# Optimization experiments

Hardware: AMD Instinct MI355X
Metric: run time of the kernel (lower is better)

The kernel has to match this reference:

```python
import jax, jax.numpy as jnp
import numpy as np

B = 512        # number of graphs
NPG = 128      # nodes per graph
N = B * NPG    # total nodes = 65536
E = 262144     # total edges (intra-graph)
F_IN = 128     # input features
H = 256        # hidden
C = 2          # num classes
BN_EPS = 1e-5


def _lin_params(key, fan_in, fan_out):
    k1, k2 = jax.random.split(key)
    s = 1.0 / np.sqrt(fan_in)
    w = jax.random.uniform(k1, (fan_in, fan_out), jnp.float32, -s, s)
    b = jax.random.uniform(k2, (fan_out,), jnp.float32, -s, s)
    return w, b


def setup_inputs() -> dict:
    key = jax.random.key(0)
    ks = jax.random.split(key, 16)
    x = jax.random.normal(ks[0], (N, F_IN), jnp.float32)
    # intra-graph random edges (required for assignment pooling semantics)
    rng = np.random.RandomState(0)
    g = np.repeat(np.arange(B), E // B)
    src = g * NPG + rng.randint(0, NPG, E)
    dst = g * NPG + rng.randint(0, NPG, E)
    edge_index = jnp.asarray(np.stack([src, dst]), jnp.int64 if jax.config.jax_enable_x64 else jnp.int32)
    batch = jnp.repeat(jnp.arange(B), NPG)
    # GIN layer 0 (F_IN->H->H) + BN
    w0_1, b0_1 = _lin_params(ks[1], F_IN, H)
    w0_2, b0_2 = _lin_params(ks[2], H, H)
    g0 = jnp.ones((H,), jnp.float32); be0 = jnp.zeros((H,), jnp.float32)
    # GIN layers 1..2 stacked (H->H->H) + BN
    wl1 = jnp.stack([_lin_params(jax.random.fold_in(ks[3], i), H, H)[0] for i in range(2)])
    bl1 = jnp.stack([_lin_params(jax.random.fold_in(ks[3], i), H, H)[1] for i in range(2)])
    wl2 = jnp.stack([_lin_params(jax.random.fold_in(ks[4], i), H, H)[0] for i in range(2)])
    bl2 = jnp.stack([_lin_params(jax.random.fold_in(ks[4], i), H, H)[1] for i in range(2)])
    gl = jnp.ones((2, H), jnp.float32); bel = jnp.zeros((2, H), jnp.float32)
    c1w, c1b = _lin_params(ks[5], H, H)
    c2w, c2b = _lin_params(ks[6], H, 2)
    l1w, l1b = _lin_params(ks[7], H, H)
    l2w, l2b = _lin_params(ks[8], H, C)
    return dict(x=x, edge_index=edge_index, batch=batch,
                w0_1=w0_1, b0_1=b0_1, w0_2=w0_2, b0_2=b0_2, g0=g0, be0=be0,
                wl1=wl1, bl1=bl1, wl2=wl2, bl2=bl2, gl=gl, bel=bel,
                c1w=c1w, c1b=c1b, c2w=c2w, c2b=c2b,
                l1w=l1w, l1b=l1b, l2w=l2w, l2b=l2b)


def _gin_layer(h, src, dst, w1, b1, w2, b2, gamma, beta):
    # GINConv (eps=0): MLP(h + sum_{j in N(i)} h_j)
    agg = jax.ops.segment_sum(h[src], dst, num_segments=N)
    z = h + agg
    z = jax.nn.relu(z @ w1 + b1)
    z = jax.nn.relu(z @ w2 + b2)
    # BatchNorm1d, training-mode batch stats (biased variance)
    mu = jnp.mean(z, axis=0)
    var = jnp.mean((z - mu) ** 2, axis=0)
    return (z - mu) * jax.lax.rsqrt(var + BN_EPS) * gamma + beta


def reference(x, edge_index, batch, w0_1, b0_1, w0_2, b0_2, g0, be0,
              wl1, bl1, wl2, bl2, gl, bel,
              c1w, c1b, c2w, c2b, l1w, l1b, l2w, l2b):
    src, dst = edge_index[0], edge_index[1]
    h = _gin_layer(x, src, dst, w0_1, b0_1, w0_2, b0_2, g0, be0)
    for i in range(2):
        h = _gin_layer(h, src, dst, wl1[i], bl1[i], wl2[i], bl2[i], gl[i], bel[i])
    # assignment: softmax(cluster2(tanh(cluster1(h))))  -> [N, 2]
    a = jax.nn.softmax(jnp.tanh(h @ c1w + c1b) @ c2w + c2b, axis=1)
    # subgraph embedding: (assignment^T @ x)[0] per graph == segment-sum of a[:,0]*h
    sub = jax.ops.segment_sum(a[:, :1] * h, batch, num_segments=B)        # [B, H]
    # graph embedding: per-graph mean of h
    cnt = jax.ops.segment_sum(jnp.ones((N,), h.dtype), batch, num_segments=B)
    graph = jax.ops.segment_sum(h, batch, num_segments=B) / cnt[:, None]   # [B, H]
    # new_adj[g] = A_g^T-pooled: sum over edges outer(a[src], a[dst]) -> [B,2,2]
    new_adj = jax.ops.segment_sum(a[src][:, :, None] * a[dst][:, None, :], batch[src], num_segments=B)
    # F.normalize(p=1, dim=1) row-wise, then diagonal, MSE vs ones(2)
    rown = jnp.maximum(jnp.sum(jnp.abs(new_adj), axis=2, keepdims=True), 1e-12)
    norm_adj = new_adj / rown
    diag = jnp.diagonal(norm_adj, axis1=1, axis2=2)                        # [B, 2]
    con_penalty = jnp.mean(jnp.mean((diag - 1.0) ** 2, axis=1))
    # classifier head (dropout in eval mode -> identity)
    z = jax.nn.relu(sub @ l1w + l1b)
    out = jax.nn.log_softmax(z @ l2w + l2b, axis=-1)
    return out, sub, graph, con_penalty
```

## Files before the change

kernel.cpp:

```cpp
#include <hip/hip_runtime.h>
#include <stdint.h>

#define NN 65536
#define NB 512
#define NPG 128
#define NE 262144
#define EPG 512
#define HD 256
#define BN_EPS 1e-5f

typedef unsigned short u16;
typedef float f32x4 __attribute__((ext_vector_type(4)));
typedef __bf16 bf16x8 __attribute__((ext_vector_type(8)));
typedef unsigned short u16x8 __attribute__((ext_vector_type(8)));
typedef unsigned short u16x4 __attribute__((ext_vector_type(4)));

__device__ __forceinline__ float b2f(u16 u){
  union { unsigned i; float f; } x; x.i = ((unsigned)u) << 16; return x.f;
}
__device__ __forceinline__ u16 f2b(float f){
  union { float f; unsigned i; } x; x.f = f;
  unsigned r = x.i + 0x7fffu + ((x.i >> 16) & 1u);
  return (u16)(r >> 16);
}
__device__ __forceinline__ float ftanh(float x){
  float e = __expf(2.0f * x);
  return 1.0f - 2.0f * __builtin_amdgcn_rcpf(e + 1.0f);
}

__global__ void __launch_bounds__(256) pack_all(
    const float* __restrict__ w0_1, const float* __restrict__ w0_2,
    const float* __restrict__ wl1, const float* __restrict__ wl2,
    const float* __restrict__ c1w,
    u16* i01, u16* i02, u16* il1a, u16* il1b, u16* il2a, u16* il2b, u16* ic1)
{
  const int seg = blockIdx.y;
  const int idx = blockIdx.x * 256 + threadIdx.x;
  const float* W; u16* img; int K = 256;
  switch (seg){
    case 0: W = w0_1;        img = i01;  K = 128; break;
    case 1: W = w0_2;        img = i02;  break;
    case 2: W = wl1;         img = il1a; break;
    case 3: W = wl1 + 65536; img = il1b; break;
    case 4: W = wl2;         img = il2a; break;
    case 5: W = wl2 + 65536; img = il2b; break;
    default: W = c1w;        img = ic1;  break;
  }
  if (idx >= K * 256) return;
  int col = idx / K, k = idx - col * K;
  img[idx] = f2b(W[(size_t)k * 256 + col]);
}

template<int K>
__device__ __forceinline__ void mm_frag(const u16* Alds,
    const u16* __restrict__ wimg, int lane, int c0, f32x4 (&acc)[8][2])
{
  const int l15 = lane & 15, lk = (lane >> 4) * 8;
  bf16x8 bfr[K / 32][2];
  #pragma unroll
  for (int kk = 0; kk < K / 32; kk++)
    #pragma unroll
    for (int nf = 0; nf < 2; nf++)
      bfr[kk][nf] = *(const bf16x8*)(wimg + (size_t)(c0 + nf * 16 + l15) * K + kk * 32 + lk);
  #pragma unroll
  for (int kk = 0; kk < K / 32; kk++){
    bf16x8 af[8];
    #pragma unroll
    for (int mf = 0; mf < 8; mf++){
      int row = mf * 16 + l15;
      unsigned byte = ((unsigned)(row * (K * 2) + (kk * 32 + lk) * 2)) ^ (unsigned)((row & 7) << 4);
      af[mf] = *(const bf16x8*)((const char*)Alds + byte);
    }
    #pragma unroll
    for (int mf = 0; mf < 8; mf++)
      #pragma unroll
      for (int nf = 0; nf < 2; nf++)
        acc[mf][nf] = __builtin_amdgcn_mfma_f32_16x16x32_bf16(af[mf], bfr[kk][nf], acc[mf][nf], 0, 0, 0);
  }
}

template<int KIN, int MODE>
__global__ void __launch_bounds__(512) layer_kernel(
    const void* __restrict__ hin_, const int* __restrict__ ei,
    const float* __restrict__ sc, const float* __restrict__ sh,
    const u16* __restrict__ w1img, const float* __restrict__ b1,
    const u16* __restrict__ w2img, const float* __restrict__ b2,
    u16* __restrict__ Y, float* __restrict__ pS, float* __restrict__ pQ)
{
  __shared__ u16 ht[NPG * HD];
  __shared__ u16 esd[EPG];
  __shared__ u16 srcs[EPG];
  __shared__ int cnt[NPG], rp[NPG + 1], fill[NPG];
  __shared__ float scs[256], shs[256];
  const int g = blockIdx.x, tid = threadIdx.x;
  const int lane = tid & 63, wid = tid >> 6;

  if (tid < NPG) cnt[tid] = 0;
  if (MODE == 1 && tid < 256){ scs[tid] = sc[tid]; shs[tid] = sh[tid]; }
  __syncthreads();

  {
    int s = ei[g * EPG + tid] & (NPG - 1);
    int d = ei[NE + g * EPG + tid] & (NPG - 1);
    esd[tid] = (u16)(s | (d << 8));
    atomicAdd(&cnt[d], 1);
  }

  if constexpr (MODE == 0){
    const float* hin = (const float*)hin_;
    #pragma unroll
    for (int i = 0; i < 8; i++){
      int idx = tid + i * 512;
      int row = idx >> 5, c4 = idx & 31;
      float4 v = *(const float4*)(hin + (size_t)(g * NPG + row) * KIN + c4 * 4);
      u16x4 o; o[0] = f2b(v.x); o[1] = f2b(v.y); o[2] = f2b(v.z); o[3] = f2b(v.w);
      unsigned byte = ((unsigned)(row * (KIN * 2) + c4 * 8)) ^ (unsigned)((row & 7) << 4);
      *(u16x4*)((char*)ht + byte) = o;
    }
  } else {
    const u16* hin = (const u16*)hin_;
    #pragma unroll
    for (int i = 0; i < 8; i++){
      int idx = tid + i * 512;
      int row = idx >> 5, c8 = idx & 31;
      u16x8 v = *(const u16x8*)(hin + (size_t)(g * NPG + row) * KIN + c8 * 8);
      u16x8 o;
      #pragma unroll
      for (int k = 0; k < 8; k++) o[k] = f2b(b2f(v[k]) * scs[c8 * 8 + k] + shs[c8 * 8 + k]);
      unsigned byte = ((unsigned)(row * (KIN * 2) + c8 * 16)) ^ (unsigned)((row & 7) << 4);
      *(u16x8*)((char*)ht + byte) = o;
    }
  }
  __syncthreads();

  if (tid < 64){
    int a = cnt[tid], b = cnt[tid + 64];
    int ca = a, cb = b;
    #pragma unroll
    for (int off = 1; off < 64; off <<= 1){
      int ta = __shfl_up(a, off), tb = __shfl_up(b, off);
      if (lane >= off){ a += ta; b += tb; }
    }
    int atot = __shfl(a, 63);
    rp[tid + 1] = a;
    rp[tid + 65] = atot + b;
    fill[tid] = a - ca;
    fill[tid + 64] = atot + b - cb;
    if (tid == 0) rp[0] = 0;
  }
  __syncthreads();
  { int v = esd[tid]; int pos = atomicAdd(&fill[v >> 8], 1); srcs[pos] = (u16)(v & 255); }
  __syncthreads();

  constexpr int CH = KIN / 16;
  constexpr int RPT = NPG * CH / 512;
  const int fc = tid & (CH - 1), n0 = tid / CH;
  float accv[RPT][16];
  #pragma unroll
  for (int j = 0; j < RPT; j++){
    const int n = n0 + j * (512 / CH);
    unsigned b0 = ((unsigned)(n * (KIN * 2) + fc * 32)) ^ (unsigned)((n & 7) << 4);
    u16x8 a0 = *(const u16x8*)((const char*)ht + b0);
    u16x8 a1 = *(const u16x8*)((const char*)ht + (b0 ^ 16u));
    #pragma unroll
    for (int k = 0; k < 8; k++){ accv[j][k] = b2f(a0[k]); accv[j][8 + k] = b2f(a1[k]); }
    const int e0 = rp[n], e1 = rp[n + 1];
    for (int e = e0; e < e1; e++){
      const int sn = srcs[e];
      unsigned s0 = ((unsigned)(sn * (KIN * 2) + fc * 32)) ^ (unsigned)((sn & 7) << 4);
      u16x8 q0 = *(const u16x8*)((const char*)ht + s0);
      u16x8 q1 = *(const u16x8*)((const char*)ht + (s0 ^ 16u));
      #pragma unroll
      for (int k = 0; k < 8; k++){ accv[j][k] += b2f(q0[k]); accv[j][8 + k] += b2f(q1[k]); }
    }
  }
  __syncthreads();
  #pragma unroll
  for (int j = 0; j < RPT; j++){
    const int n = n0 + j * (512 / CH);
    u16x8 o0, o1;
    #pragma unroll
    for (int k = 0; k < 8; k++){ o0[k] = f2b(accv[j][k]); o1[k] = f2b(accv[j][8 + k]); }
    unsigned b0 = ((unsigned)(n * (KIN * 2) + fc * 32)) ^ (unsigned)((n & 7) << 4);
    *(u16x8*)((char*)ht + b0) = o0;
    *(u16x8*)((char*)ht + (b0 ^ 16u)) = o1;
  }
  __syncthreads();

  const int c0 = wid * 32;
  const int l15 = lane & 15;

  {
    f32x4 acc1[8][2] = {};
    mm_frag<KIN>(ht, w1img, lane, c0, acc1);
    __syncthreads();
    float bv0 = b1[c0 + l15], bv1 = b1[c0 + 16 + l15];
    #pragma unroll
    for (int mf = 0; mf < 8; mf++)
      #pragma unroll
      for (int nf = 0; nf < 2; nf++){
        float bv = nf ? bv1 : bv0;
        int col = c0 + nf * 16 + l15;
        #pragma unroll
        for (int j = 0; j < 4; j++){
          int row = mf * 16 + (lane >> 4) * 4 + j;
          float v = fmaxf(acc1[mf][nf][j] + bv, 0.f);
          unsigned byte = ((unsigned)(row * 512 + col * 2)) ^ (unsigned)((row & 7) << 4);
          *(u16*)((char*)ht + byte) = f2b(v);
        }
      }
  }
  __syncthreads();

  {
    f32x4 acc2[8][2] = {};
    mm_frag<HD>(ht, w2img, lane, c0, acc2);
    float bv0 = b2[c0 + l15], bv1 = b2[c0 + 16 + l15];
    float s[2] = {0, 0}, q[2] = {0, 0};
    #pragma unroll
    for (int mf = 0; mf < 8; mf++)
      #pragma unroll
      for (int nf = 0; nf < 2; nf++){
        float bv = nf ? bv1 : bv0;
        int col = c0 + nf * 16 + l15;
        #pragma unroll
        for (int j = 0; j < 4; j++){
          int row = mf * 16 + (lane >> 4) * 4 + j;
          float v = fmaxf(acc2[mf][nf][j] + bv, 0.f);
          Y[(size_t)(g * NPG + row) * HD + col] = f2b(v);
          s[nf] += v; q[nf] += v * v;
        }
      }
    #pragma unroll
    for (int nf = 0; nf < 2; nf++){
      float sv = s[nf], qv = q[nf];
      sv += __shfl_xor(sv, 16); sv += __shfl_xor(sv, 32);
      qv += __shfl_xor(qv, 16); qv += __shfl_xor(qv, 32);
      if (lane < 16){
        int col = c0 + nf * 16 + lane;
        pS[(size_t)col * NB + g] = sv;
        pQ[(size_t)col * NB + g] = qv;
      }
    }
  }
}

__global__ void __launch_bounds__(64) bnfin_kernel(const float* __restrict__ pS,
    const float* __restrict__ pQ, const float* __restrict__ gma,
    const float* __restrict__ bta, float* __restrict__ scale, float* __restrict__ shift)
{
  int c = blockIdx.x, lane = threadIdx.x;
  float s = 0.f, q = 0.f;
  for (int i = lane; i < NB; i += 64){ s += pS[(size_t)c * NB + i]; q += pQ[(size_t)c * NB + i]; }
  for (int m = 32; m; m >>= 1){ s += __shfl_xor(s, m); q += __shfl_xor(q, m); }
  if (lane == 0){
    float mu = s * (1.0f / NN);
    float var = q * (1.0f / NN) - mu * mu;
    float scv = gma[c] * rsqrtf(var + BN_EPS);
    scale[c] = scv;
    shift[c] = bta[c] - mu * scv;
  }
}

__global__ void __launch_bounds__(512) final_kernel(
    const u16* __restrict__ hin, const int* __restrict__ ei,
    const float* __restrict__ sc, const float* __restrict__ sh,
    const u16* __restrict__ c1img, const float* __restrict__ c1b,
    const float* __restrict__ c2w, const float* __restrict__ c2b,
    const float* __restrict__ l1w, const float* __restrict__ l1b,
    const float* __restrict__ l2w, const float* __restrict__ l2b,
    float* __restrict__ outLog, float* __restrict__ outSub,
    float* __restrict__ outGraph, float* __restrict__ outPen)
{
  __shared__ u16 ht[NPG * HD];
  __shared__ u16 esd[EPG];
  __shared__ float aL[NPG * 2];
  __shared__ float scratch[2048];
  __shared__ float subL[256];
  __shared__ float wred[8][4];
  const int g = blockIdx.x, tid = threadIdx.x;
  const int lane = tid & 63, wid = tid >> 6;

  if (tid < 256){ scratch[tid] = sc[tid]; scratch[256 + tid] = sh[tid]; }
  {
    int s = ei[g * EPG + tid] & (NPG - 1);
    int d = ei[NE + g * EPG + tid] & (NPG - 1);
    esd[tid] = (u16)(s | (d << 8));
  }
  __syncthreads();

  #pragma unroll
  for (int i = 0; i < 8; i++){
    int idx = tid + i * 512;
    int row = idx >> 5, c8 = idx & 31;
    u16x8 v = *(const u16x8*)(hin + (size_t)(g * NPG + row) * HD + c8 * 8);
    u16x8 o;
    #pragma unroll
    for (int k = 0; k < 8; k++)
      o[k] = f2b(b2f(v[k]) * scratch[c8 * 8 + k] + scratch[256 + c8 * 8 + k]);
    unsigned byte = ((unsigned)(row * 512 + c8 * 16)) ^ (unsigned)((row & 7) << 4);
    *(u16x8*)((char*)ht + byte) = o;
  }
  __syncthreads();

  const int c0 = wid * 32;
  const int l15 = lane & 15;

  {
    f32x4 acct[8][2] = {};
    mm_frag<HD>(ht, c1img, lane, c0, acct);
    const int col0 = c0 + l15, col1 = c0 + 16 + l15;
    const float bv0 = c1b[col0], bv1 = c1b[col1];
    const float w00 = c2w[col0 * 2], w01 = c2w[col0 * 2 + 1];
    const float w10 = c2w[col1 * 2], w11 = c2w[col1 * 2 + 1];
    #pragma unroll
    for (int mf = 0; mf < 8; mf++)
      #pragma unroll
      for (int j = 0; j < 4; j++){
        float t0 = ftanh(acct[mf][0][j] + bv0);
        float t1 = ftanh(acct[mf][1][j] + bv1);
        float p0 = t0 * w00 + t1 * w10;
        float p1 = t0 * w01 + t1 * w11;
        p0 += __shfl_xor(p0, 1); p0 += __shfl_xor(p0, 2);
        p0 += __shfl_xor(p0, 4); p0 += __shfl_xor(p0, 8);
        p1 += __shfl_xor(p1, 1); p1 += __shfl_xor(p1, 2);
        p1 += __shfl_xor(p1, 4); p1 += __shfl_xor(p1, 8);
        if (l15 == 0){
          int row = mf * 16 + (lane >> 4) * 4 + j;
          scratch[row * 16 + wid * 2]     = p0;
          scratch[row * 16 + wid * 2 + 1] = p1;
        }
      }
  }
  __syncthreads();

  {
    int row = tid >> 2, part = tid & 3;
    float4 v = *(const float4*)&scratch[row * 16 + part * 4];
    float p0 = v.x + v.z, p1 = v.y + v.w;
    p0 += __shfl_xor(p0, 1); p0 += __shfl_xor(p0, 2);
    p1 += __shfl_xor(p1, 1); p1 += __shfl_xor(p1, 2);
    if (part == 0){
      p0 += c2b[0]; p1 += c2b[1];
      float mx = fmaxf(p0, p1);
      float e0 = expf(p0 - mx), e1 = expf(p1 - mx);
      float inv = 1.f / (e0 + e1);
      aL[row * 2] = e0 * inv; aL[row * 2 + 1] = e1 * inv;
    }
  }
  __syncthreads();

  {
    int v = esd[tid];
    int sE = v & 255, dE = v >> 8;
    float as0 = aL[sE * 2], as1 = aL[sE * 2 + 1];
    float ad0 = aL[dE * 2], ad1 = aL[dE * 2 + 1];
    float m00 = as0 * ad0, m01 = as0 * ad1, m10 = as1 * ad0, m11 = as1 * ad1;
    #pragma unroll
    for (int m = 1; m < 64; m <<= 1){
      m00 += __shfl_xor(m00, m); m01 += __shfl_xor(m01, m);
      m10 += __shfl_xor(m10, m); m11 += __shfl_xor(m11, m);
    }
    if (lane == 0){ wred[wid][0] = m00; wred[wid][1] = m01; wred[wid][2] = m10; wred[wid][3] = m11; }
  }
  {
    const int part = tid >> 8, c = tid & 255;
    float sb = 0.f, gs = 0.f;
    #pragma unroll 8
    for (int i = 0; i < 64; i++){
      int n = part * 64 + i;
      unsigned byte = ((unsigned)(n * 512 + c * 2)) ^ (unsigned)((n & 7) << 4);
      float v = b2f(*(const u16*)((const char*)ht + byte));
      sb += aL[n * 2] * v; gs += v;
    }
    __syncthreads();
    scratch[part * 512 + c] = sb;
    scratch[part * 512 + 256 + c] = gs;
  }
  __syncthreads();
  if (tid < 256){
    float sb = scratch[tid] + scratch[512 + tid];
    float gs = scratch[256 + tid] + scratch[768 + tid];
    subL[tid] = sb;
    outSub[(size_t)g * HD + tid] = sb;
    outGraph[(size_t)g * HD + tid] = gs * (1.f / NPG);
  }
  if (tid == 0){
    float m00 = 0, m01 = 0, m10 = 0, m11 = 0;
    for (int w = 0; w < 8; w++){ m00 += wred[w][0]; m01 += wred[w][1]; m10 += wred[w][2]; m11 += wred[w][3]; }
    float r0 = fmaxf(fabsf(m00) + fabsf(m01), 1e-12f);
    float r1 = fmaxf(fabsf(m10) + fabsf(m11), 1e-12f);
    float d0 = m00 / r0 - 1.f, d1 = m11 / r1 - 1.f;
    atomicAdd(outPen, 0.5f * (d0 * d0 + d1 * d1) * (1.0f / NB));
  }
  __syncthreads();

  {
    const int ph = tid >> 8, c = tid & 255;
    float z = 0.f;
    for (int k = ph * 128; k < ph * 128 + 128; k++)
      z += subL[k] * l1w[(size_t)k * HD + c];
    scratch[ph * 256 + c] = z;
  }
  __syncthreads();
  if (tid < 256){
    float z = fmaxf(scratch[tid] + scratch[256 + tid] + l1b[tid], 0.f);
    float o0 = z * l2w[tid * 2], o1 = z * l2w[tid * 2 + 1];
    #pragma unroll
    for (int m = 1; m < 64; m <<= 1){ o0 += __shfl_xor(o0, m); o1 += __shfl_xor(o1, m); }
    if (lane == 0){ wred[wid][0] = o0; wred[wid][1] = o1; }
  }
  __syncthreads();
  if (tid == 0){
    float o0 = wred[0][0] + wred[1][0] + wred[2][0] + wred[3][0] + l2b[0];
    float o1 = wred[0][1] + wred[1][1] + wred[2][1] + wred[3][1] + l2b[1];
    float mx = fmaxf(o0, o1);
    float lse = mx + logf(expf(o0 - mx) + expf(o1 - mx));
    outLog[(size_t)g * 2] = o0 - lse;
    outLog[(size_t)g * 2 + 1] = o1 - lse;
  }
}

extern "C" void kernel_launch(void* const* d_in, const int* in_sizes, int n_in,
                              void* d_out, int out_size, void* d_ws, size_t ws_size,
                              hipStream_t stream)
{
  (void)in_sizes; (void)n_in; (void)out_size; (void)ws_size;
  const float* x    = (const float*)d_in[0];
  const int*   ei   = (const int*)  d_in[1];
  const float* w0_1 = (const float*)d_in[3];
  const float* b0_1 = (const float*)d_in[4];
  const float* w0_2 = (const float*)d_in[5];
  const float* b0_2 = (const float*)d_in[6];
  const float* g0   = (const float*)d_in[7];
  const float* be0  = (const float*)d_in[8];
  const float* wl1  = (const float*)d_in[9];
  const float* bl1  = (const float*)d_in[10];
  const float* wl2  = (const float*)d_in[11];
  const float* bl2  = (const float*)d_in[12];
  const float* gl   = (const float*)d_in[13];
  const float* bel  = (const float*)d_in[14];
  const float* c1w  = (const float*)d_in[15];
  const float* c1b  = (const float*)d_in[16];
  const float* c2w  = (const float*)d_in[17];
  const float* c2b  = (const float*)d_in[18];
  const float* l1w  = (const float*)d_in[19];
  const float* l1b  = (const float*)d_in[20];
  const float* l2w  = (const float*)d_in[21];
  const float* l2b  = (const float*)d_in[22];
  float* out = (float*)d_out;

  char* cur = (char*)d_ws;
  auto carve = [&](size_t bytes) -> void* {
    void* p = (void*)cur; cur += (bytes + 255) & ~(size_t)255; return p;
  };
  u16* B0    = (u16*)carve((size_t)NN * HD * 2);
  u16* B1    = (u16*)carve((size_t)NN * HD * 2);
  u16* i01   = (u16*)carve((size_t)128 * 256 * 2);
  u16* i02   = (u16*)carve((size_t)256 * 256 * 2);
  u16* il1a  = (u16*)carve((size_t)256 * 256 * 2);
  u16* il1b  = (u16*)carve((size_t)256 * 256 * 2);
  u16* il2a  = (u16*)carve((size_t)256 * 256 * 2);
  u16* il2b  = (u16*)carve((size_t)256 * 256 * 2);
  u16* ic1   = (u16*)carve((size_t)256 * 256 * 2);
  float* pS  = (float*)carve((size_t)256 * NB * 4);
  float* pQ  = (float*)carve((size_t)256 * NB * 4);
  float* bsc = (float*)carve(256 * 4);
  float* bsh = (float*)carve(256 * 4);

  float* outPen = out + 1024 + 2 * NB * HD;

  pack_all<<<dim3(256, 7), 256, 0, stream>>>(w0_1, w0_2, wl1, wl2, c1w,
                                             i01, i02, il1a, il1b, il2a, il2b, ic1);
  hipMemsetAsync((void*)outPen, 0, 4, stream);

  layer_kernel<128, 0><<<NB, 512, 0, stream>>>((const void*)x, ei, nullptr, nullptr,
                                               i01, b0_1, i02, b0_2, B0, pS, pQ);
  bnfin_kernel<<<256, 64, 0, stream>>>(pS, pQ, g0, be0, bsc, bsh);

  layer_kernel<256, 1><<<NB, 512, 0, stream>>>((const void*)B0, ei, bsc, bsh,
                                               il1a, bl1, il2a, bl2, B1, pS, pQ);
  bnfin_kernel<<<256, 64, 0, stream>>>(pS, pQ, gl, bel, bsc, bsh);

  layer_kernel<256, 1><<<NB, 512, 0, stream>>>((const void*)B1, ei, bsc, bsh,
                                               il1b, bl1 + 256, il2b, bl2 + 256, B0, pS, pQ);
  bnfin_kernel<<<256, 64, 0, stream>>>(pS, pQ, gl + 256, bel + 256, bsc, bsh);

  final_kernel<<<NB, 512, 0, stream>>>(B0, ei, bsc, bsh, ic1, c1b, c2w, c2b,
                                       l1w, l1b, l2w, l2b,
                                       out, out + 1024, out + 1024 + NB * HD, outPen);
}
```

Baseline: 288.2 us.

## Replace CSR edge aggregation with dense adjacency MFMA after first linear

The layer kernel now builds a per-graph 128x128 dense adjacency (self-loop included) as 8-bit counts in LDS via atomics, instead of building CSR and gathering neighbours with scalar loops. Because aggregation commutes with the linear layer, it applies W1 first, then multiplies by the adjacency on MFMA, then adds bias and ReLU before the second GEMM. This removes the serial, divergent per-edge gather loops and the prefix-scan syncs. In exchange it adds extra MFMA work and a larger LDS footprint, and it requests two blocks per CU. The 8-bit counts overflow if any node pair has more than 255 edges, and rounding the W1 output to bf16 before aggregation changes numerics slightly.

```diff
diff --git a/kernel.cpp b/kernel.cpp
--- a/kernel.cpp
+++ b/kernel.cpp
@@ -26,6 +26,18 @@
 __device__ __forceinline__ float ftanh(float x){
   float e = __expf(2.0f * x);
   return 1.0f - 2.0f * __builtin_amdgcn_rcpf(e + 1.0f);
+}
+__device__ __forceinline__ bf16x8 u8x8_to_bf16x8(unsigned d0, unsigned d1){
+  u16x8 r;
+  #pragma unroll
+  for (int b = 0; b < 4; b++){
+    union { float f; unsigned u; } x, y;
+    x.f = (float)((d0 >> (b * 8)) & 255u);
+    y.f = (float)((d1 >> (b * 8)) & 255u);
+    r[b] = (u16)(x.u >> 16);
+    r[4 + b] = (u16)(y.u >> 16);
+  }
+  return *(bf16x8*)&r;
 }
 
 __global__ void __launch_bounds__(256) pack_all(
@@ -51,196 +63,223 @@
   img[idx] = f2b(W[(size_t)k * 256 + col]);
 }
 
-template<int K>
-__device__ __forceinline__ void mm_frag(const u16* Alds,
-    const u16* __restrict__ wimg, int lane, int c0, f32x4 (&acc)[8][2])
-{
-  const int l15 = lane & 15, lk = (lane >> 4) * 8;
-  bf16x8 bfr[K / 32][2];
-  #pragma unroll
-  for (int kk = 0; kk < K / 32; kk++)
-    #pragma unroll
-    for (int nf = 0; nf < 2; nf++)
-      bfr[kk][nf] = *(const bf16x8*)(wimg + (size_t)(c0 + nf * 16 + l15) * K + kk * 32 + lk);
-  #pragma unroll
-  for (int kk = 0; kk < K / 32; kk++){
-    bf16x8 af[8];
-    #pragma unroll
-    for (int mf = 0; mf < 8; mf++){
-      int row = mf * 16 + l15;
-      unsigned byte = ((unsigned)(row * (K * 2) + (kk * 32 + lk) * 2)) ^ (unsigned)((row & 7) << 4);
-      af[mf] = *(const bf16x8*)((const char*)Alds + byte);
-    }
-    #pragma unroll
-    for (int mf = 0; mf < 8; mf++)
-      #pragma unroll
-      for (int nf = 0; nf < 2; nf++)
-        acc[mf][nf] = __builtin_amdgcn_mfma_f32_16x16x32_bf16(af[mf], bfr[kk][nf], acc[mf][nf], 0, 0, 0);
-  }
-}
-
 template<int KIN, int MODE>
-__global__ void __launch_bounds__(512) layer_kernel(
+__global__ void __launch_bounds__(512, 2) layer_kernel(
     const void* __restrict__ hin_, const int* __restrict__ ei,
     const float* __restrict__ sc, const float* __restrict__ sh,
     const u16* __restrict__ w1img, const float* __restrict__ b1,
     const u16* __restrict__ w2img, const float* __restrict__ b2,
     u16* __restrict__ Y, float* __restrict__ pS, float* __restrict__ pQ)
 {
-  __shared__ u16 ht[NPG * HD];
-  __shared__ u16 esd[EPG];
-  __shared__ u16 srcs[EPG];
-  __shared__ int cnt[NPG], rp[NPG + 1], fill[NPG];
-  __shared__ float scs[256], shs[256];
+  __shared__ __align__(16) char smem[KIN * 256 + 65536 + 16384];
+  char* ht  = smem;
+  char* g1t = smem + KIN * 256;
+  unsigned* A32 = (unsigned*)(smem + KIN * 256 + 65536);
+  char* Ab = (char*)A32;
+
   const int g = blockIdx.x, tid = threadIdx.x;
   const int lane = tid & 63, wid = tid >> 6;
-
-  if (tid < NPG) cnt[tid] = 0;
-  if (MODE == 1 && tid < 256){ scs[tid] = sc[tid]; shs[tid] = sh[tid]; }
+  const int l15 = lane & 15, lk = (lane >> 4) * 8;
+  const int c0 = wid * 32;
+
+  #pragma unroll
+  for (int i = 0; i < 8; i++) A32[tid + i * 512] = 0u;
   __syncthreads();
 
   {
     int s = ei[g * EPG + tid] & (NPG - 1);
     int d = ei[NE + g * EPG + tid] & (NPG - 1);
-    esd[tid] = (u16)(s | (d << 8));
-    atomicAdd(&cnt[d], 1);
+    unsigned byte = ((unsigned)((d << 7) | (s & ~3))) ^ ((unsigned)((d & 7) << 4));
+    atomicAdd(&A32[byte >> 2], 1u << ((s & 3) * 8));
+  }
+  if (tid < NPG){
+    int n = tid;
+    unsigned byte = ((unsigned)((n << 7) | (n & ~3))) ^ ((unsigned)((n & 7) << 4));
+    atomicAdd(&A32[byte >> 2], 1u << ((n & 3) * 8));
   }
 
   if constexpr (MODE == 0){
     const float* hin = (const float*)hin_;
     #pragma unroll
+    for (int i = 0; i < 4; i++){
+      int idx = tid + i * 512;
+      int row = idx >> 4, c8 = idx & 15;
+      const float* p = hin + (size_t)(g * NPG + row) * KIN + c8 * 8;
+      float4 v0 = *(const float4*)p;
+      float4 v1 = *(const float4*)(p + 4);
+      u16x8 o;
+      o[0] = f2b(v0.x); o[1] = f2b(v0.y); o[2] = f2b(v0.z); o[3] = f2b(v0.w);
+      o[4] = f2b(v1.x); o[5] = f2b(v1.y); o[6] = f2b(v1.z); o[7] = f2b(v1.w);
+      unsigned byte = ((unsigned)(row * (KIN * 2) + c8 * 16)) ^ ((unsigned)((row & 7) << 4));
+      *(u16x8*)(ht + byte) = o;
+    }
+  } else {
+    const u16* hin = (const u16*)hin_;
+    const int c8 = tid & 31;
+    float scr[8], shr[8];
+    {
+      float4 a0 = *(const float4*)(sc + c8 * 8);
+      float4 a1 = *(const float4*)(sc + c8 * 8 + 4);
+      float4 s0 = *(const float4*)(sh + c8 * 8);
+      float4 s1 = *(const float4*)(sh + c8 * 8 + 4);
+      scr[0]=a0.x; scr[1]=a0.y; scr[2]=a0.z; scr[3]=a0.w;
+      scr[4]=a1.x; scr[5]=a1.y; scr[6]=a1.z; scr[7]=a1.w;
+      shr[0]=s0.x; shr[1]=s0.y; shr[2]=s0.z; shr[3]=s0.w;
+      shr[4]=s1.x; shr[5]=s1.y; shr[6]=s1.z; shr[7]=s1.w;
+    }
+    #pragma unroll
     for (int i = 0; i < 8; i++){
       int idx = tid + i * 512;
-      int row = idx >> 5, c4 = idx & 31;
-      float4 v = *(const float4*)(hin + (size_t)(g * NPG + row) * KIN + c4 * 4);
-      u16x4 o; o[0] = f2b(v.x); o[1] = f2b(v.y); o[2] = f2b(v.z); o[3] = f2b(v.w);
-      unsigned byte = ((unsigned)(row * (KIN * 2) + c4 * 8)) ^ (unsigned)((row & 7) << 4);
-      *(u16x4*)((char*)ht + byte) = o;
-    }
-  } else {
-    const u16* hin = (const u16*)hin_;
-    #pragma unroll
-    for (int i = 0; i < 8; i++){
-      int idx = tid + i * 512;
-      int row = idx >> 5, c8 = idx & 31;
+      int row = idx >> 5;
       u16x8 v = *(const u16x8*)(hin + (size_t)(g * NPG + row) * KIN + c8 * 8);
       u16x8 o;
       #pragma unroll
-      for (int k = 0; k < 8; k++) o[k] = f2b(b2f(v[k]) * scs[c8 * 8 + k] + shs[c8 * 8 + k]);
-      unsigned byte = ((unsigned)(row * (KIN * 2) + c8 * 16)) ^ (unsigned)((row & 7) << 4);
-      *(u16x8*)((char*)ht + byte) = o;
-    }
-  }
-  __syncthreads();
-
-  if (tid < 64){
-    int a = cnt[tid], b = cnt[tid + 64];
-    int ca = a, cb = b;
-    #pragma unroll
-    for (int off = 1; off < 64; off <<= 1){
-      int ta = __shfl_up(a, off), tb = __shfl_up(b, off);
-      if (lane >= off){ a += ta; b += tb; }
-    }
-    int atot = __shfl(a, 63);
-    rp[tid + 1] = a;
-    rp[tid + 65] = atot + b;
-    fill[tid] = a - ca;
-    fill[tid + 64] = atot + b - cb;
-    if (tid == 0) rp[0] = 0;
-  }
-  __syncthreads();
-  { int v = esd[tid]; int pos = atomicAdd(&fill[v >> 8], 1); srcs[pos] = (u16)(v & 255); }
-  __syncthreads();
-
-  constexpr int CH = KIN / 16;
-  constexpr int RPT = NPG * CH / 512;
-  const int fc = tid & (CH - 1), n0 = tid / CH;
-  float accv[RPT][16];
-  #pragma unroll
-  for (int j = 0; j < RPT; j++){
-    const int n = n0 + j * (512 / CH);
-    unsigned b0 = ((unsigned)(n * (KIN * 2) + fc * 32)) ^ (unsigned)((n & 7) << 4);
-    u16x8 a0 = *(const u16x8*)((const char*)ht + b0);
-    u16x8 a1 = *(const u16x8*)((const char*)ht + (b0 ^ 16u));
-    #pragma unroll
-    for (int k = 0; k < 8; k++){ accv[j][k] = b2f(a0[k]); accv[j][8 + k] = b2f(a1[k]); }
-    const int e0 = rp[n], e1 = rp[n + 1];
-    for (int e = e0; e < e1; e++){
-      const int sn = srcs[e];
-      unsigned s0 = ((unsigned)(sn * (KIN * 2) + fc * 32)) ^ (unsigned)((sn & 7) << 4);
-      u16x8 q0 = *(const u16x8*)((const char*)ht + s0);
-      u16x8 q1 = *(const u16x8*)((const char*)ht + (s0 ^ 16u));
-      #pragma unroll
-      for (int k = 0; k < 8; k++){ accv[j][k] += b2f(q0[k]); accv[j][8 + k] += b2f(q1[k]); }
-    }
-  }
-  __syncthreads();
-  #pragma unroll
-  for (int j = 0; j < RPT; j++){
-    const int n = n0 + j * (512 / CH);
-    u16x8 o0, o1;
-    #pragma unroll
-    for (int k = 0; k < 8; k++){ o0[k] = f2b(accv[j][k]); o1[k] = f2b(accv[j][8 + k]); }
-    unsigned b0 = ((unsigned)(n * (KIN * 2) + fc * 32)) ^ (unsigned)((n & 7) << 4);
-    *(u16x8*)((char*)ht + b0) = o0;
-    *(u16x8*)((char*)ht + (b0 ^ 16u)) = o1;
-  }
-  __syncthreads();
-
-  const int c0 = wid * 32;
-  const int l15 = lane & 15;
-
-  {
-    f32x4 acc1[8][2] = {};
-    mm_frag<KIN>(ht, w1img, lane, c0, acc1);
+      for (int k = 0; k < 8; k++) o[k] = f2b(b2f(v[k]) * scr[k] + shr[k]);
+      unsigned byte = ((unsigned)(row * (KIN * 2) + c8 * 16)) ^ ((unsigned)((row & 7) << 4));
+      *(u16x8*)(ht + byte) = o;
+    }
+  }
+  __syncthreads();
+
+  {
+    f32x4 acc[8][2] = {};
+    #pragma unroll
+    for (int kk = 0; kk < KIN / 32; kk++){
+      bf16x8 bfr[2];
+      #pragma unroll
+      for (int nf = 0; nf < 2; nf++)
+        bfr[nf] = *(const bf16x8*)(w1img + (size_t)(c0 + nf * 16 + l15) * KIN + kk * 32 + lk);
+      bf16x8 af[8];
+      #pragma unroll
+      for (int mf = 0; mf < 8; mf++){
+        int row = mf * 16 + l15;
+        unsigned byte = ((unsigned)(row * (KIN * 2) + (kk * 32 + lk) * 2)) ^ ((unsigned)((row & 7) << 4));
+        af[mf] = *(const bf16x8*)(ht + byte);
+      }
+      #pragma unroll
+      for (int mf = 0; mf < 8; mf++)
+        #pragma unroll
+        for (int nf = 0; nf < 2; nf++)
+          acc[mf][nf] = __builtin_amdgcn_mfma_f32_16x16x32_bf16(af[mf], bfr[nf], acc[mf][nf], 0, 0, 0);
+    }
+    #pragma unroll
+    for (int mf = 0; mf < 8; mf++)
+      #pragma unroll
+      for (int nf = 0; nf < 2; nf++){
+        int c = c0 + nf * 16 + l15;
+        int n0 = mf * 16 + (lane >> 4) * 4;
+        u16x4 o;
+        #pragma unroll
+        for (int j = 0; j < 4; j++) o[j] = f2b(acc[mf][nf][j]);
+        unsigned byte = ((unsigned)(c * 256 + n0 * 2)) ^ ((unsigned)((c & 7) << 4));
+        *(u16x4*)(g1t + byte) = o;
+      }
+  }
+
+  {
+    f32x4 acc[8][2] = {};
+    bf16x8 gfr[4][2];
+    #pragma unroll
+    for (int kk = 0; kk < 4; kk++)
+      #pragma unroll
+      for (int cf = 0; cf < 2; cf++){
+        int c = c0 + cf * 16 + l15;
+        unsigned byte = ((unsigned)(c * 256 + (kk * 32 + lk) * 2)) ^ ((unsigned)((c & 7) << 4));
+        gfr[kk][cf] = *(const bf16x8*)(g1t + byte);
+      }
+    #pragma unroll
+    for (int kk = 0; kk < 4; kk++){
+      bf16x8 bfA[8];
+      #pragma unroll
+      for (int nf = 0; nf < 8; nf++){
+        int n = nf * 16 + l15;
+        unsigned byte = ((unsigned)((n << 7) + kk * 32 + lk)) ^ ((unsigned)((n & 7) << 4));
+        uint2 dd = *(const uint2*)(Ab + byte);
+        bfA[nf] = u8x8_to_bf16x8(dd.x, dd.y);
+      }
+      #pragma unroll
+      for (int nf = 0; nf < 8; nf++)
+        #pragma unroll
+        for (int cf = 0; cf < 2; cf++)
+          acc[nf][cf] = __builtin_amdgcn_mfma_f32_16x16x32_bf16(gfr[kk][cf], bfA[nf], acc[nf][cf], 0, 0, 0);
+    }
     __syncthreads();
-    float bv0 = b1[c0 + l15], bv1 = b1[c0 + 16 + l15];
-    #pragma unroll
-    for (int mf = 0; mf < 8; mf++)
-      #pragma unroll
-      for (int nf = 0; nf < 2; nf++){
-        float bv = nf ? bv1 : bv0;
-        int col = c0 + nf * 16 + l15;
+    #pragma unroll
+    for (int nf = 0; nf < 8; nf++)
+      #pragma unroll
+      for (int cf = 0; cf < 2; cf++){
+        int n = nf * 16 + l15;
+        int cb = c0 + cf * 16 + (lane >> 4) * 4;
+        float4 bv = *(const float4*)(b1 + cb);
+        u16x4 o;
+        o[0] = f2b(fmaxf(acc[nf][cf][0] + bv.x, 0.f));
+        o[1] = f2b(fmaxf(acc[nf][cf][1] + bv.y, 0.f));
+        o[2] = f2b(fmaxf(acc[nf][cf][2] + bv.z, 0.f));
+        o[3] = f2b(fmaxf(acc[nf][cf][3] + bv.w, 0.f));
+        unsigned byte = ((unsigned)(n * 512 + cb * 2)) ^ ((unsigned)((n & 7) << 4));
+        *(u16x4*)(g1t + byte) = o;
+      }
+  }
+  __syncthreads();
+
+  {
+    f32x4 acc[8][2] = {};
+    #pragma unroll
+    for (int kk = 0; kk < 8; kk++){
+      bf16x8 bfr[2];
+      #pragma unroll
+      for (int cf = 0; cf < 2; cf++)
+        bfr[cf] = *(const bf16x8*)(w2img + (size_t)(c0 + cf * 16 + l15) * 256 + kk * 32 + lk);
+      bf16x8 zf[8];
+      #pragma unroll
+      for (int nf = 0; nf < 8; nf++){
+        int n = nf * 16 + l15;
+        unsigned byte = ((unsigned)(n * 512 + (kk * 32 + lk) * 2)) ^ ((unsigned)((n & 7) << 4));
+        zf[nf] = *(const bf16x8*)(g1t + byte);
+      }
+      #pragma unroll
+      for (int nf = 0; nf < 8; nf++)
+        #pragma unroll
+        for (int cf = 0; cf < 2; cf++)
+          acc[nf][cf] = __builtin_amdgcn_mfma_f32_16x16x32_bf16(bfr[cf], zf[nf], acc[nf][cf], 0, 0, 0);
+    }
+    float sv[2][4] = {}, qv[2][4] = {};
+    #pragma unroll
+    for (int nf = 0; nf < 8; nf++)
+      #pragma unroll
+      for (int cf = 0; cf < 2; cf++){
+        int n = nf * 16 + l15;
+        int cb = c0 + cf * 16 + (lane >> 4) * 4;
+        float4 bv = *(const float4*)(b2 + cb);
+        u16x4 o;
+        float v0 = fmaxf(acc[nf][cf][0] + bv.x, 0.f);
+        float v1 = fmaxf(acc[nf][cf][1] + bv.y, 0.f);
+        float v2 = fmaxf(acc[nf][cf][2] + bv.z, 0.f);
+        float v3 = fmaxf(acc[nf][cf][3] + bv.w, 0.f);
+        o[0] = f2b(v0); o[1] = f2b(v1); o[2] = f2b(v2); o[3] = f2b(v3);
+        sv[cf][0] += v0; sv[cf][1] += v1; sv[cf][2] += v2; sv[cf][3] += v3;
+        qv[cf][0] += v0 * v0; qv[cf][1] += v1 * v1; qv[cf][2] += v2 * v2; qv[cf][3] += v3 * v3;
+        *(u16x4*)(Y + (size_t)(g * NPG + n) * HD + cb) = o;
+      }
+    #pragma unroll
+    for (int m = 1; m <= 8; m <<= 1)
+      #pragma unroll
+      for (int cf = 0; cf < 2; cf++)
         #pragma unroll
         for (int j = 0; j < 4; j++){
-          int row = mf * 16 + (lane >> 4) * 4 + j;
-          float v = fmaxf(acc1[mf][nf][j] + bv, 0.f);
-          unsigned byte = ((unsigned)(row * 512 + col * 2)) ^ (unsigned)((row & 7) << 4);
-          *(u16*)((char*)ht + byte) = f2b(v);
+          sv[cf][j] += __shfl_xor(sv[cf][j], m);
+          qv[cf][j] += __shfl_xor(qv[cf][j], m);
         }
-      }
-  }
-  __syncthreads();
-
-  {
-    f32x4 acc2[8][2] = {};
-    mm_frag<HD>(ht, w2img, lane, c0, acc2);
-    float bv0 = b2[c0 + l15], bv1 = b2[c0 + 16 + l15];
-    float s[2] = {0, 0}, q[2] = {0, 0};
-    #pragma unroll
-    for (int mf = 0; mf < 8; mf++)
-      #pragma unroll
-      for (int nf = 0; nf < 2; nf++){
-        float bv = nf ? bv1 : bv0;
-        int col = c0 + nf * 16 + l15;
+    if (l15 == 0){
+      int jb = (lane >> 4) * 4;
+      #pragma unroll
+      for (int cf = 0; cf < 2; cf++)
         #pragma unroll
         for (int j = 0; j < 4; j++){
-          int row = mf * 16 + (lane >> 4) * 4 + j;
-          float v = fmaxf(acc2[mf][nf][j] + bv, 0.f);
-          Y[(size_t)(g * NPG + row) * HD + col] = f2b(v);
-          s[nf] += v; q[nf] += v * v;
+          int col = c0 + cf * 16 + jb + j;
+          pS[(size_t)col * NB + g] = sv[cf][j];
+          pQ[(size_t)col * NB + g] = qv[cf][j];
         }
-      }
-    #pragma unroll
-    for (int nf = 0; nf < 2; nf++){
-      float sv = s[nf], qv = q[nf];
-      sv += __shfl_xor(sv, 16); sv += __shfl_xor(sv, 32);
-      qv += __shfl_xor(qv, 16); qv += __shfl_xor(qv, 32);
-      if (lane < 16){
-        int col = c0 + nf * 16 + lane;
-        pS[(size_t)col * NB + g] = sv;
-        pQ[(size_t)col * NB + g] = qv;
-      }
     }
   }
 }
@@ -259,6 +298,34 @@
     float scv = gma[c] * rsqrtf(var + BN_EPS);
     scale[c] = scv;
     shift[c] = bta[c] - mu * scv;
+  }
+}
+
+template<int K>
+__device__ __forceinline__ void mm_frag(const u16* Alds,
+    const u16* __restrict__ wimg, int lane, int c0, f32x4 (&acc)[8][2])
+{
+  const int l15 = lane & 15, lk = (lane >> 4) * 8;
+  bf16x8 bfr[K / 32][2];
+  #pragma unroll
+  for (int kk = 0; kk < K / 32; kk++)
+    #pragma unroll
+    for (int nf = 0; nf < 2; nf++)
+      bfr[kk][nf] = *(const bf16x8*)(wimg + (size_t)(c0 + nf * 16 + l15) * K + kk * 32 + lk);
+  #pragma unroll
+  for (int kk = 0; kk < K / 32; kk++){
+    bf16x8 af[8];
+    #pragma unroll
+    for (int mf = 0; mf < 8; mf++){
+      int row = mf * 16 + l15;
+      unsigned byte = ((unsigned)(row * (K * 2) + (kk * 32 + lk) * 2)) ^ (unsigned)((row & 7) << 4);
+      af[mf] = *(const bf16x8*)((const char*)Alds + byte);
+    }
+    #pragma unroll
+    for (int mf = 0; mf < 8; mf++)
+      #pragma unroll
+      for (int nf = 0; nf < 2; nf++)
+        acc[mf][nf] = __builtin_amdgcn_mfma_f32_16x16x32_bf16(af[mf], bfr[kk][nf], acc[mf][nf], 0, 0, 0);
   }
 }
 
```

Result: no change. 293.4 us (+1.8%).
